# Optimization experiments

Measured on AMD Instinct MI355X. Metric: run time of the kernel, lower is better.

## Reference

```python
import jax, jax.numpy as jnp
import numpy as np
from jax.scipy.special import logsumexp

EPS = 1e-12  # torch F.normalize eps
SINKHORN_ITERS = 3


def _l2norm(a, axis):
    n = jnp.sqrt(jnp.sum(a * a, axis=axis, keepdims=True))
    return a / jnp.maximum(n, EPS)


def _log_optimal_transport(scores, alpha, iters):
    # scores: [B, m, n]; alpha: scalar dust-bin param
    b, m, n = scores.shape
    bins = jnp.broadcast_to(alpha, (b, 1, n)).astype(scores.dtype)
    Z = jnp.concatenate([scores, bins], axis=1)  # [B, m+1, n]
    norm = -np.log(float(m + n))
    log_mu = jnp.asarray(
        np.concatenate([np.full(m, norm), [np.log(float(n - m)) + norm]]),
        scores.dtype,
    )  # [m+1]
    log_nu = jnp.full((n,), norm, scores.dtype)
    u = jnp.zeros((b, m + 1), scores.dtype)
    v = jnp.zeros((b, n), scores.dtype)
    for _ in range(iters):
        u = log_mu[None, :] - logsumexp(Z + v[:, None, :], axis=2)
        v = log_nu[None, :] - logsumexp(Z + u[:, :, None], axis=1)
    return Z + u[:, :, None] + v[:, None, :] - norm


def _forward(x, t, tw1, tb1, tw2, tb2, cw1, cb1, cw2, cb2, sw1, sb1, sw2, sb2, dust_bin):
    B, C = x.shape[0], x.shape[1]
    xf = x.reshape(B, C, -1)  # [B, C, N], 1x1 convs act per-location
    # cluster features f: [B, l, N]
    h = jax.nn.relu(jnp.einsum('oc,bcn->bon', cw1, xf) + cb1[None, :, None])
    f = jnp.einsum('oc,bcn->bon', cw2, h) + cb2[None, :, None]
    # global token: [B, g]
    tok = jax.nn.relu(t @ tw1.T + tb1) @ tw2.T + tb2
    # assignment scores p: [B, m, N]
    hs = jax.nn.relu(jnp.einsum('oc,bcn->bon', sw1, xf) + sb1[None, :, None])
    p = jnp.einsum('oc,bcn->bon', sw2, hs) + sb2[None, :, None]
    Z = _log_optimal_transport(p, dust_bin, SINKHORN_ITERS)
    P = jnp.exp(Z)[:, :-1, :]  # drop dust bin row -> [B, m, N]
    # VLAD-style aggregation: the repeat/multiply/sum is just a batched matmul
    agg = jnp.einsum('bln,bmn->blm', f, P)  # [B, l, m]
    agg = _l2norm(agg, axis=1).reshape(B, -1)  # intra-normalize over l, flatten l-major
    out = jnp.concatenate([_l2norm(tok, axis=-1), agg], axis=-1)
    return _l2norm(out, axis=-1)


def setup_inputs() -> dict:
    key = jax.random.key(0)
    ks = jax.random.split(key, 14)
    B, C, H, W = 64, 768, 32, 32
    L, M, G, HID = 128, 64, 256, 512

    def p(k, shape):
        return jax.random.normal(k, shape, jnp.float32) * 0.02

    return {
        'x': jax.random.normal(ks[0], (B, C, H, W), jnp.float32),
        't': jax.random.normal(ks[1], (B, C), jnp.float32),
        'tw1': p(ks[2], (HID, C)), 'tb1': jnp.zeros((HID,), jnp.float32),
        'tw2': p(ks[3], (G, HID)), 'tb2': jnp.zeros((G,), jnp.float32),
        'cw1': p(ks[4], (HID, C)), 'cb1': jnp.zeros((HID,), jnp.float32),
        'cw2': p(ks[5], (L, HID)), 'cb2': jnp.zeros((L,), jnp.float32),
        'sw1': p(ks[6], (HID, C)), 'sb1': jnp.zeros((HID,), jnp.float32),
        'sw2': p(ks[7], (M, HID)), 'sb2': jnp.zeros((M,), jnp.float32),
        'dust_bin': jnp.asarray(1.0, jnp.float32),
    }


def reference(x, t, tw1, tb1, tw2, tb2, cw1, cb1, cw2, cb2, sw1, sb1, sw2, sb2, dust_bin):
    return _forward(x, t, tw1, tb1, tw2, tb2, cw1, cb1, cw2, cb2, sw1, sb1, sw2, sb2, dust_bin)
```

## Files before the change

### kernel.cpp

```cpp
#include <hip/hip_runtime.h>
#include <math.h>


#define B_SZ   64
#define C_IN   768
#define N_LOC  1024
#define HID    512
#define L_DIM  128
#define M_DIM  64
#define G_DIM  256

typedef unsigned short u16;
typedef __bf16 bf16x8 __attribute__((ext_vector_type(8)));
typedef float f32x4 __attribute__((ext_vector_type(4)));

typedef const __attribute__((address_space(1))) void* gptr_t;
typedef __attribute__((address_space(3))) void* sptr_t;

__device__ __forceinline__ void load_lds16(const void* g, void* l) {
    __builtin_amdgcn_global_load_lds((gptr_t)g, (sptr_t)l, 16, 0, 0);
}

__device__ __forceinline__ u16 f2bf(float f) {
    unsigned u = __float_as_uint(f);
    u += 0x7fffu + ((u >> 16) & 1u);
    return (u16)(u >> 16);
}
__device__ __forceinline__ float bf2f(u16 h) {
    return __uint_as_float(((unsigned)h) << 16);
}

__device__ __forceinline__ float waveReduceSum(float v) {
#pragma unroll
    for (int off = 32; off > 0; off >>= 1) v += __shfl_xor(v, off, 64);
    return v;
}

__global__ __launch_bounds__(256) void prep_weights(
        const float* __restrict__ cw1, const float* __restrict__ sw1,
        const float* __restrict__ cw2, const float* __restrict__ sw2,
        u16* __restrict__ cw1p, u16* __restrict__ sw1p,
        u16* __restrict__ cw2p, u16* __restrict__ sw2p) {
    const int q = blockIdx.x * 256 + threadIdx.x;
    const float* src;
    u16* dst;
    if (q < 98304) {
        int path = q / 49152, r = q % 49152;
        int kch = r / 512, c = r & 511;
        src = (path ? sw1 : cw1) + (size_t)c * C_IN + kch * 8;
        dst = (path ? sw1p : cw1p) + (size_t)r * 8;
    } else {
        int q2 = q - 98304;
        int path = (q2 >= 8192) ? 1 : 0;
        int r = q2 - (path ? 8192 : 0);
        int S2 = path ? M_DIM : L_DIM;
        int k2 = r / (4 * S2), kc = (r / S2) & 3, c = r % S2;
        src = (path ? sw2 : cw2) + (size_t)c * HID + k2 * 32 + kc * 8;
        dst = (path ? sw2p : cw2p) + (size_t)r * 8;
    }
    float4 v0 = *(const float4*)(src);
    float4 v1 = *(const float4*)(src + 4);
    *(ushort4*)(dst) = make_ushort4(f2bf(v0.x), f2bf(v0.y), f2bf(v0.z), f2bf(v0.w));
    *(ushort4*)(dst + 4) = make_ushort4(f2bf(v1.x), f2bf(v1.y), f2bf(v1.z), f2bf(v1.w));
}

__global__ __launch_bounds__(256) void transpose_x(const float* __restrict__ x,
                                                   u16* __restrict__ xP) {
    __shared__ float tile[64][65];
    const int n0 = blockIdx.x * 64;
    const int c0 = blockIdx.y * 64;
    const size_t b = blockIdx.z;
    const float* xb = x + b * (size_t)(C_IN * N_LOC);
    u16* xpb = xP + b * (size_t)(N_LOC * C_IN);
    const int tid = threadIdx.x;

    const int jn = (tid & 15) * 4;
    const int cr = tid >> 4;
#pragma unroll
    for (int r = 0; r < 4; ++r) {
        int c = cr + r * 16;
        float4 v = *(const float4*)(xb + (size_t)(c0 + c) * N_LOC + n0 + jn);
        tile[c][jn + 0] = v.x;
        tile[c][jn + 1] = v.y;
        tile[c][jn + 2] = v.z;
        tile[c][jn + 3] = v.w;
    }
    __syncthreads();

    const int n = tid & 63;
    const int ch0 = tid >> 6;
    const int nG = n0 + n;
#pragma unroll
    for (int r = 0; r < 2; ++r) {
        const int ch = ch0 + r * 4;
        const int cG = c0 + ch * 8;
        u16* dst = xpb + (size_t)(nG >> 7) * (128 * C_IN) + (cG >> 3) * 1024 +
                   (nG & 127) * 8;
        ushort4 o0 = make_ushort4(f2bf(tile[ch * 8 + 0][n]), f2bf(tile[ch * 8 + 1][n]),
                                  f2bf(tile[ch * 8 + 2][n]), f2bf(tile[ch * 8 + 3][n]));
        ushort4 o1 = make_ushort4(f2bf(tile[ch * 8 + 4][n]), f2bf(tile[ch * 8 + 5][n]),
                                  f2bf(tile[ch * 8 + 6][n]), f2bf(tile[ch * 8 + 7][n]));
        *(ushort4*)(dst) = o0;
        *(ushort4*)(dst + 4) = o1;
    }
}

__global__ __launch_bounds__(512, 2) void fused12(
        const u16* __restrict__ xP,
        const u16* __restrict__ cw1p, const float* __restrict__ cb1,
        const u16* __restrict__ cw2p, const float* __restrict__ cb2,
        const u16* __restrict__ sw1p, const float* __restrict__ sb1,
        const u16* __restrict__ sw2p, const float* __restrict__ sb2,
        u16* __restrict__ fT, u16* __restrict__ pT) {
    __shared__ __align__(16) u16 LDSu[81920];
    const int tid = threadIdx.x;
    const int lane = tid & 63;
    const int wid = tid >> 6;
    const int wr = wid >> 2;
    const int wc = wid & 3;

    const int id = blockIdx.x + 8 * blockIdx.y + 16 * blockIdx.z;
    const int nid = (id & 7) * 128 + (id >> 3);
    const int bx = nid & 7;
    const int path = (nid >> 3) & 1;
    const int bz = nid >> 4;
    const int r0 = bx * 128;

    const u16* W1p = path ? sw1p : cw1p;
    const float* B1 = path ? sb1 : cb1;
    const u16* W2p = path ? sw2p : cw2p;
    const float* B2 = path ? sb2 : cb2;
    u16* O2 = path ? pT : fT;
    const int S2 = path ? M_DIM : L_DIM;

    const u16* Ap = xP + (size_t)bz * N_LOC * C_IN + (size_t)bx * (128 * C_IN);

    f32x4 acc1[4][8];
#pragma unroll
    for (int mi = 0; mi < 4; ++mi)
#pragma unroll
        for (int ni = 0; ni < 8; ++ni)
            acc1[mi][ni] = (f32x4){0.f, 0.f, 0.f, 0.f};

    const int nk = C_IN / 64;

#define STG_A(db_, kt_)                                                        \
    do {                                                                       \
        _Pragma("unroll")                                                      \
        for (int j_ = 0; j_ < 2; ++j_)                                         \
            load_lds16(Ap + (size_t)(kt_) * 8192 + (size_t)(j_ * 512 + tid) * 8, \
                       &LDSu[(db_) * 8192 + (j_ * 512 + tid) * 8]);            \
    } while (0)
#define STG_B(db_, kt_)                                                        \
    do {                                                                       \
        _Pragma("unroll")                                                      \
        for (int j_ = 0; j_ < 8; ++j_)                                         \
            load_lds16(W1p + (size_t)(kt_) * 32768 + (size_t)(j_ * 512 + tid) * 8, \
                       &LDSu[16384 + (db_) * 32768 + (j_ * 512 + tid) * 8]);   \
    } while (0)

#define AV_PTR(db_, kk_, mi_)                                                  \
    ((const bf16x8*)&LDSu[(db_) * 8192 + ((kk_) * 4 + (lane >> 4)) * 1024 +    \
                          (64 * wr + 16 * (mi_) + (lane & 15)) * 8])
#define BW_PTR(db_, kk_, ni_)                                                  \
    ((const bf16x8*)&LDSu[16384 + (db_) * 32768 +                              \
                          ((kk_) * 4 + (lane >> 4)) * 4096 +                   \
                          (128 * wc + 16 * (ni_) + (lane & 15)) * 8])

#define PHASE_MID()                                                            \
    __builtin_amdgcn_s_barrier();                                              \
    asm volatile("s_waitcnt lgkmcnt(0)" ::: "memory");                         \
    __builtin_amdgcn_sched_barrier(0);                                         \
    __builtin_amdgcn_s_setprio(1)

#define PHASE_END()                                                            \
    __builtin_amdgcn_s_setprio(0);                                             \
    __builtin_amdgcn_sched_barrier(0);                                         \
    __builtin_amdgcn_s_barrier()

    STG_A(0, 0);
    STG_B(0, 0);
    asm volatile("s_waitcnt vmcnt(0)" ::: "memory");
    __builtin_amdgcn_s_barrier();

    for (int t = 0; t < nk; ++t) {
        const int db = t & 1;
        bf16x8 av[4], bw[8];

#pragma unroll
        for (int mi = 0; mi < 4; ++mi) av[mi] = *AV_PTR(db, 0, mi);
#pragma unroll
        for (int ni = 0; ni < 8; ++ni) bw[ni] = *BW_PTR(db, 0, ni);
        if (t + 1 < nk) {
            STG_B(db ^ 1, t + 1);
            STG_A(db ^ 1, t + 1);
        }
        PHASE_MID();
#pragma unroll
        for (int mi = 0; mi < 4; ++mi)
#pragma unroll
            for (int ni = 0; ni < 8; ++ni)
                acc1[mi][ni] = __builtin_amdgcn_mfma_f32_16x16x32_bf16(
                    av[mi], bw[ni], acc1[mi][ni], 0, 0, 0);
        PHASE_END();

#pragma unroll
        for (int mi = 0; mi < 4; ++mi) av[mi] = *AV_PTR(db, 1, mi);
#pragma unroll
        for (int ni = 0; ni < 8; ++ni) bw[ni] = *BW_PTR(db, 1, ni);
        PHASE_MID();
#pragma unroll
        for (int mi = 0; mi < 4; ++mi)
#pragma unroll
            for (int ni = 0; ni < 8; ++ni)
                acc1[mi][ni] = __builtin_amdgcn_mfma_f32_16x16x32_bf16(
                    av[mi], bw[ni], acc1[mi][ni], 0, 0, 0);
        __builtin_amdgcn_s_setprio(0);
        __builtin_amdgcn_sched_barrier(0);
        asm volatile("s_waitcnt vmcnt(0)" ::: "memory");
        __builtin_amdgcn_s_barrier();
    }
#undef STG_A
#undef STG_B
#undef AV_PTR
#undef BW_PTR
#undef PHASE_MID
#undef PHASE_END

    {
        float bv1[8];
#pragma unroll
        for (int ni = 0; ni < 8; ++ni)
            bv1[ni] = B1[128 * wc + 16 * ni + (lane & 15)];
#pragma unroll
        for (int mi = 0; mi < 4; ++mi)
#pragma unroll
            for (int ni = 0; ni < 8; ++ni)
#pragma unroll
                for (int rr = 0; rr < 4; ++rr) {
                    int n = 64 * wr + 16 * mi + (lane >> 4) * 4 + rr;
                    int c = 128 * wc + 16 * ni + (lane & 15);
                    float v = fmaxf(acc1[mi][ni][rr] + bv1[ni], 0.f);
                    LDSu[(c >> 3) * 1024 + n * 8 + (c & 7)] = f2bf(v);
                }
    }
    __syncthreads();

    f32x4 acc2[4][2];
#pragma unroll
    for (int mi = 0; mi < 4; ++mi) {
        acc2[mi][0] = (f32x4){0.f, 0.f, 0.f, 0.f};
        acc2[mi][1] = (f32x4){0.f, 0.f, 0.f, 0.f};
    }
    const int c2base = (S2 == L_DIM) ? 32 * wc : 16 * wc;
    const int cA = c2base + (lane & 15);
    const int cB = c2base + 16 + (lane & 15);
    const int fb0 = (lane >> 4) * S2 + cA;
    const int fb1 = (lane >> 4) * S2 + cB;

    bf16x8 w0n = *(const bf16x8*)(W2p + (size_t)fb0 * 8);
    bf16x8 w1n = {};
    if (S2 == L_DIM) w1n = *(const bf16x8*)(W2p + (size_t)fb1 * 8);

    for (int k2 = 0; k2 < 16; ++k2) {
        bf16x8 w0 = w0n, w1 = w1n;
        if (k2 < 15) {
            w0n = *(const bf16x8*)(W2p + ((size_t)(k2 + 1) * 4 * S2 + fb0) * 8);
            if (S2 == L_DIM)
                w1n = *(const bf16x8*)(W2p + ((size_t)(k2 + 1) * 4 * S2 + fb1) * 8);
        }
        bf16x8 a2[4];
#pragma unroll
        for (int mi = 0; mi < 4; ++mi)
            a2[mi] = *(const bf16x8*)&LDSu[(k2 * 4 + (lane >> 4)) * 1024 +
                                           (64 * wr + 16 * mi + (lane & 15)) * 8];
#pragma unroll
        for (int mi = 0; mi < 4; ++mi) {
            acc2[mi][0] = __builtin_amdgcn_mfma_f32_16x16x32_bf16(
                a2[mi], w0, acc2[mi][0], 0, 0, 0);
            if (S2 == L_DIM)
                acc2[mi][1] = __builtin_amdgcn_mfma_f32_16x16x32_bf16(
                    a2[mi], w1, acc2[mi][1], 0, 0, 0);
        }
    }

    const float b20 = B2[cA];
    const float b21 = (S2 == L_DIM) ? B2[cB] : 0.f;
    u16* Ob = O2 + (size_t)bz * N_LOC * S2;
#pragma unroll
    for (int mi = 0; mi < 4; ++mi)
#pragma unroll
        for (int rr = 0; rr < 4; ++rr) {
            int row = r0 + 64 * wr + 16 * mi + (lane >> 4) * 4 + rr;
            Ob[(size_t)row * S2 + cA] = f2bf(acc2[mi][0][rr] + b20);
            if (S2 == L_DIM)
                Ob[(size_t)row * S2 + cB] = f2bf(acc2[mi][1][rr] + b21);
        }
}

__global__ __launch_bounds__(256) void tok1_kernel(const float* __restrict__ t,
                                                   const float* __restrict__ tw1,
                                                   const float* __restrict__ tb1,
                                                   float* __restrict__ hidb) {
    __shared__ __align__(16) float tl[C_IN];
    const int b = blockIdx.y;
    const int j0 = blockIdx.x * 64;
    const int tid = threadIdx.x;
    const int lane = tid & 63;
    const int wave = tid >> 6;
    for (int i = tid; i < C_IN; i += 256) tl[i] = t[(size_t)b * C_IN + i];
    __syncthreads();
    for (int j = wave; j < 64; j += 4) {
        const int row = j0 + j;
        const float4* wr = (const float4*)(tw1 + (size_t)row * C_IN);
        const float4* tr = (const float4*)tl;
        float s = 0.f;
#pragma unroll
        for (int q = 0; q < 3; ++q) {
            float4 wv = wr[lane + 64 * q];
            float4 tv = tr[lane + 64 * q];
            s += wv.x * tv.x + wv.y * tv.y + wv.z * tv.z + wv.w * tv.w;
        }
        s = waveReduceSum(s);
        if (lane == 0) hidb[(size_t)b * HID + row] = fmaxf(s + tb1[row], 0.f);
    }
}

__global__ __launch_bounds__(256) void tok2_kernel(const float* __restrict__ hidb,
                                                   const float* __restrict__ tw2,
                                                   const float* __restrict__ tb2,
                                                   float* __restrict__ tok) {
    __shared__ __align__(16) float hl[HID];
    const int b = blockIdx.y;
    const int g0 = blockIdx.x * 64;
    const int tid = threadIdx.x;
    const int lane = tid & 63;
    const int wave = tid >> 6;
    for (int i = tid; i < HID; i += 256) hl[i] = hidb[(size_t)b * HID + i];
    __syncthreads();
    for (int j = wave; j < 64; j += 4) {
        const int row = g0 + j;
        const float4* wr = (const float4*)(tw2 + (size_t)row * HID);
        const float4* hr = (const float4*)hl;
        float s = 0.f;
#pragma unroll
        for (int q = 0; q < 2; ++q) {
            float4 wv = wr[lane + 64 * q];
            float4 hv = hr[lane + 64 * q];
            s += wv.x * hv.x + wv.y * hv.y + wv.z * hv.z + wv.w * hv.w;
        }
        s = waveReduceSum(s);
        if (lane == 0) tok[(size_t)b * G_DIM + row] = s + tb2[row];
    }
}

__global__ __launch_bounds__(1024) void sinkhorn_kernel(const u16* __restrict__ pT,
                                                        const float* __restrict__ dust,
                                                        float* __restrict__ PT) {
    __shared__ u16 sp[M_DIM][N_LOC];
    __shared__ float eu[M_DIM + 1];
    __shared__ float ev[N_LOC];
    const int b = blockIdx.x;
    const int t = threadIdx.x;
    const int lane = t & 63;
    const int wave = t >> 6;
    const float alpha = dust[0];
    const float Ea = __expf(alpha);
    const float mu = 1.f / 1088.f;
    const float mu64 = 960.f / 1088.f;
    const float nu = 1.f / 1088.f;

    const uint4* prow = (const uint4*)(pT + ((size_t)b * N_LOC + t) * M_DIM);
#pragma unroll
    for (int q = 0; q < 8; ++q) {
        uint4 ch = prow[q];
        sp[q * 8 + 0][t] = (u16)(ch.x);
        sp[q * 8 + 1][t] = (u16)(ch.x >> 16);
        sp[q * 8 + 2][t] = (u16)(ch.y);
        sp[q * 8 + 3][t] = (u16)(ch.y >> 16);
        sp[q * 8 + 4][t] = (u16)(ch.z);
        sp[q * 8 + 5][t] = (u16)(ch.z >> 16);
        sp[q * 8 + 6][t] = (u16)(ch.w);
        sp[q * 8 + 7][t] = (u16)(ch.w >> 16);
    }
#pragma unroll
    for (int m = 0; m < M_DIM; ++m)
        sp[m][t] = f2bf(__expf(bf2f(sp[m][t])));
    ev[t] = 1.f;
    __syncthreads();

    for (int it = 0; it < 3; ++it) {
        for (int m = wave; m < M_DIM + 1; m += 16) {
            float s = 0.f;
            if (m < M_DIM) {
#pragma unroll
                for (int q = 0; q < 16; ++q) {
                    int c = lane + 64 * q;
                    s += bf2f(sp[m][c]) * ev[c];
                }
            } else {
#pragma unroll
                for (int q = 0; q < 16; ++q) {
                    int c = lane + 64 * q;
                    s += ev[c];
                }
                s *= Ea;
            }
            s = waveReduceSum(s);
            if (lane == 0) eu[m] = ((m < M_DIM) ? mu : mu64) / s;
        }
        __syncthreads();
        float s = Ea * eu[M_DIM];
#pragma unroll 8
        for (int m = 0; m < M_DIM; ++m) s += bf2f(sp[m][t]) * eu[m];
        ev[t] = nu / s;
        __syncthreads();
    }

    const float evt = ev[t] * 1088.f;
    float* Prow = PT + ((size_t)b * N_LOC + t) * M_DIM;
#pragma unroll
    for (int m4 = 0; m4 < M_DIM; m4 += 4) {
        float4 o;
        o.x = bf2f(sp[m4 + 0][t]) * eu[m4 + 0] * evt;
        o.y = bf2f(sp[m4 + 1][t]) * eu[m4 + 1] * evt;
        o.z = bf2f(sp[m4 + 2][t]) * eu[m4 + 2] * evt;
        o.w = bf2f(sp[m4 + 3][t]) * eu[m4 + 3] * evt;
        *(float4*)(Prow + m4) = o;
    }
}

__global__ __launch_bounds__(256) void agg_kernel(const u16* __restrict__ fT,
                                                  const float* __restrict__ PT,
                                                  float* __restrict__ agg) {
    __shared__ float Fs[64][36];
    __shared__ float Ps[64][68];
    const int b = blockIdx.y;
    const int l0 = blockIdx.x * 32;
    const int tid = threadIdx.x;
    const u16* fb = fT + (size_t)b * N_LOC * L_DIM;
    const float* Pb = PT + (size_t)b * N_LOC * M_DIM;

    const int sn = tid >> 2;
    const int flc = (tid & 3) * 8;
    const int pmc = (tid & 3) * 16;
    const int tl = (tid >> 4) * 2;
    const int tm = (tid & 15) * 4;

    float acc[2][4] = {};

    for (int n0 = 0; n0 < N_LOC; n0 += 64) {
        __syncthreads();
        {
            uint4 ld = *(const uint4*)(fb + (size_t)(n0 + sn) * L_DIM + l0 + flc);
            Fs[sn][flc + 0] = bf2f((u16)(ld.x));
            Fs[sn][flc + 1] = bf2f((u16)(ld.x >> 16));
            Fs[sn][flc + 2] = bf2f((u16)(ld.y));
            Fs[sn][flc + 3] = bf2f((u16)(ld.y >> 16));
            Fs[sn][flc + 4] = bf2f((u16)(ld.z));
            Fs[sn][flc + 5] = bf2f((u16)(ld.z >> 16));
            Fs[sn][flc + 6] = bf2f((u16)(ld.w));
            Fs[sn][flc + 7] = bf2f((u16)(ld.w >> 16));
        }
#pragma unroll
        for (int i = 0; i < 4; ++i) {
            float4 vv = *(const float4*)(Pb + (size_t)(n0 + sn) * M_DIM + pmc + 4 * i);
            *(float4*)&Ps[sn][pmc + 4 * i] = vv;
        }
        __syncthreads();
#pragma unroll 8
        for (int nn = 0; nn < 64; ++nn) {
            float a0 = Fs[nn][tl];
            float a1 = Fs[nn][tl + 1];
            float4 p4 = *(const float4*)&Ps[nn][tm];
            acc[0][0] = fmaf(a0, p4.x, acc[0][0]);
            acc[0][1] = fmaf(a0, p4.y, acc[0][1]);
            acc[0][2] = fmaf(a0, p4.z, acc[0][2]);
            acc[0][3] = fmaf(a0, p4.w, acc[0][3]);
            acc[1][0] = fmaf(a1, p4.x, acc[1][0]);
            acc[1][1] = fmaf(a1, p4.y, acc[1][1]);
            acc[1][2] = fmaf(a1, p4.z, acc[1][2]);
            acc[1][3] = fmaf(a1, p4.w, acc[1][3]);
        }
    }

#pragma unroll
    for (int i = 0; i < 2; ++i) {
        float* dst = agg + ((size_t)b * L_DIM + l0 + tl + i) * M_DIM + tm;
        *(float4*)dst = make_float4(acc[i][0], acc[i][1], acc[i][2], acc[i][3]);
    }
}

__global__ __launch_bounds__(256) void final_kernel(const float* __restrict__ agg,
                                                    const float* __restrict__ tok,
                                                    float* __restrict__ out) {
    __shared__ __align__(16) float ag[L_DIM * M_DIM];
    __shared__ float rm[M_DIM];
    __shared__ float red[4];
    __shared__ float tk[G_DIM];
    const int b = blockIdx.x;
    const int tid = threadIdx.x;
    const int lane = tid & 63;
    const int wave = tid >> 6;
    const float EPS = 1e-12f;

    const float4* ab = (const float4*)(agg + (size_t)b * L_DIM * M_DIM);
    for (int e4 = tid; e4 < L_DIM * M_DIM / 4; e4 += 256) ((float4*)ag)[e4] = ab[e4];
    tk[tid] = tok[(size_t)b * G_DIM + tid];
    __syncthreads();

    if (tid < M_DIM) {
        float ss = 0.f;
#pragma unroll 8
        for (int l = 0; l < L_DIM; ++l) {
            float x = ag[l * M_DIM + tid];
            ss = fmaf(x, x, ss);
        }
        rm[tid] = 1.f / fmaxf(sqrtf(ss), EPS);
    }
    const float tv = tk[tid];
    float ssl = tv * tv;
    ssl = waveReduceSum(ssl);
    if (lane == 0) red[wave] = ssl;
    __syncthreads();
    const float stok = red[0] + red[1] + red[2] + red[3];
    const float rt = 1.f / fmaxf(sqrtf(stok), EPS);
    const float tn = tv * rt;

    float gs = tn * tn;
    for (int e = tid; e < L_DIM * M_DIM; e += 256) {
        float x = ag[e] * rm[e & (M_DIM - 1)];
        gs = fmaf(x, x, gs);
    }
    __syncthreads();
    gs = waveReduceSum(gs);
    if (lane == 0) red[wave] = gs;
    __syncthreads();
    const float G = red[0] + red[1] + red[2] + red[3];
    const float rg = 1.f / fmaxf(sqrtf(G), EPS);

    float* ob = out + (size_t)b * (G_DIM + L_DIM * M_DIM);
    ob[tid] = tn * rg;
    for (int e = tid; e < L_DIM * M_DIM; e += 256)
        ob[G_DIM + e] = ag[e] * rm[e & (M_DIM - 1)] * rg;
}

extern "C" void kernel_launch(void* const* d_in, const int* in_sizes, int n_in,
                              void* d_out, int out_size, void* d_ws, size_t ws_size,
                              hipStream_t stream) {
    const float* x    = (const float*)d_in[0];
    const float* t    = (const float*)d_in[1];
    const float* tw1  = (const float*)d_in[2];
    const float* tb1  = (const float*)d_in[3];
    const float* tw2  = (const float*)d_in[4];
    const float* tb2  = (const float*)d_in[5];
    const float* cw1  = (const float*)d_in[6];
    const float* cb1  = (const float*)d_in[7];
    const float* cw2  = (const float*)d_in[8];
    const float* cb2  = (const float*)d_in[9];
    const float* sw1  = (const float*)d_in[10];
    const float* sb1  = (const float*)d_in[11];
    const float* sw2  = (const float*)d_in[12];
    const float* sb2  = (const float*)d_in[13];
    const float* dust = (const float*)d_in[14];
    float* out = (float*)d_out;

    char* ws = (char*)d_ws;
    u16* xP    = (u16*)(ws);
    u16* fT    = (u16*)(ws + 100663296ull);
    u16* pT    = (u16*)(ws + 117440512ull);
    u16* cw1p  = (u16*)(ws + 125829120ull);
    u16* sw1p  = (u16*)(ws + 126615552ull);
    u16* cw2p  = (u16*)(ws + 127401984ull);
    u16* sw2p  = (u16*)(ws + 127533056ull);
    float* hidb = (float*)(ws + 127598592ull);
    float* PT     = (float*)(ws);
    float* tokbuf = (float*)(ws + 20971520ull);
    float* aggbuf = (float*)(ws + 25165824ull);

    prep_weights<<<432, 256, 0, stream>>>(cw1, sw1, cw2, sw2,
                                          cw1p, sw1p, cw2p, sw2p);
    transpose_x<<<dim3(N_LOC / 64, C_IN / 64, B_SZ), 256, 0, stream>>>(x, xP);

    fused12<<<dim3(8, 2, B_SZ), 512, 0, stream>>>(
        xP, cw1p, cb1, cw2p, cb2, sw1p, sb1, sw2p, sb2, fT, pT);

    tok1_kernel<<<dim3(HID / 64, B_SZ), 256, 0, stream>>>(t, tw1, tb1, hidb);
    tok2_kernel<<<dim3(G_DIM / 64, B_SZ), 256, 0, stream>>>(hidb, tw2, tb2, tokbuf);

    sinkhorn_kernel<<<B_SZ, 1024, 0, stream>>>(pT, dust, PT);
    agg_kernel<<<dim3(L_DIM / 32, B_SZ), 256, 0, stream>>>(fT, PT, aggbuf);
    final_kernel<<<B_SZ, 256, 0, stream>>>(aggbuf, tokbuf, out);
}
```

Before: 291.5 us.

## Shrink first GEMM K-tile with triple-buffered A and store transport plan as bf16

The first fused GEMM stage now uses K-tiles of 32 instead of 64, with a smaller LDS footprint. The activation tile is prefetched two steps ahead while the weight tile is double-buffered, and the loop uses one barrier pair per step instead of two phases. Separately, the Sinkhorn kernel writes the transport plan in bf16 instead of fp32, halving that intermediate's traffic into the aggregation kernel. The risks are more loop iterations and barriers per K, plus reduced precision in the transport plan.

```diff
diff --git a/kernel.cpp b/kernel.cpp
--- a/kernel.cpp
+++ b/kernel.cpp
@@ -112,7 +112,7 @@
         const u16* __restrict__ sw1p, const float* __restrict__ sb1,
         const u16* __restrict__ sw2p, const float* __restrict__ sb2,
         u16* __restrict__ fT, u16* __restrict__ pT) {
-    __shared__ __align__(16) u16 LDSu[81920];
+    __shared__ __align__(16) u16 LDSu[65536];
     const int tid = threadIdx.x;
     const int lane = tid & 63;
     const int wid = tid >> 6;
@@ -142,45 +142,29 @@
         for (int ni = 0; ni < 8; ++ni)
             acc1[mi][ni] = (f32x4){0.f, 0.f, 0.f, 0.f};
 
-    const int nk = C_IN / 64;
+    const int nk = C_IN / 32;
 
 #define STG_A(db_, kt_)                                                        \
-    do {                                                                       \
-        _Pragma("unroll")                                                      \
-        for (int j_ = 0; j_ < 2; ++j_)                                         \
-            load_lds16(Ap + (size_t)(kt_) * 8192 + (size_t)(j_ * 512 + tid) * 8, \
-                       &LDSu[(db_) * 8192 + (j_ * 512 + tid) * 8]);            \
-    } while (0)
+    load_lds16(Ap + (size_t)(kt_) * 4096 + tid * 8, &LDSu[(db_) * 4096 + tid * 8])
 #define STG_B(db_, kt_)                                                        \
     do {                                                                       \
         _Pragma("unroll")                                                      \
-        for (int j_ = 0; j_ < 8; ++j_)                                         \
-            load_lds16(W1p + (size_t)(kt_) * 32768 + (size_t)(j_ * 512 + tid) * 8, \
-                       &LDSu[16384 + (db_) * 32768 + (j_ * 512 + tid) * 8]);   \
+        for (int j_ = 0; j_ < 4; ++j_)                                         \
+            load_lds16(W1p + (size_t)(kt_) * 16384 + (size_t)(j_ * 512 + tid) * 8, \
+                       &LDSu[8192 + (db_) * 16384 + (j_ * 512 + tid) * 8]);    \
     } while (0)
 
-#define AV_PTR(db_, kk_, mi_)                                                  \
-    ((const bf16x8*)&LDSu[(db_) * 8192 + ((kk_) * 4 + (lane >> 4)) * 1024 +    \
+#define AV_PTR(db_, mi_)                                                       \
+    ((const bf16x8*)&LDSu[(db_) * 4096 + (lane >> 4) * 1024 +                  \
                           (64 * wr + 16 * (mi_) + (lane & 15)) * 8])
-#define BW_PTR(db_, kk_, ni_)                                                  \
-    ((const bf16x8*)&LDSu[16384 + (db_) * 32768 +                              \
-                          ((kk_) * 4 + (lane >> 4)) * 4096 +                   \
+#define BW_PTR(db_, ni_)                                                       \
+    ((const bf16x8*)&LDSu[8192 + (db_) * 16384 + (lane >> 4) * 4096 +          \
                           (128 * wc + 16 * (ni_) + (lane & 15)) * 8])
-
-#define PHASE_MID()                                                            \
-    __builtin_amdgcn_s_barrier();                                              \
-    asm volatile("s_waitcnt lgkmcnt(0)" ::: "memory");                         \
-    __builtin_amdgcn_sched_barrier(0);                                         \
-    __builtin_amdgcn_s_setprio(1)
-
-#define PHASE_END()                                                            \
-    __builtin_amdgcn_s_setprio(0);                                             \
-    __builtin_amdgcn_sched_barrier(0);                                         \
-    __builtin_amdgcn_s_barrier()
 
     STG_A(0, 0);
     STG_B(0, 0);
-    asm volatile("s_waitcnt vmcnt(0)" ::: "memory");
+    STG_A(1, 1);
+    asm volatile("s_waitcnt vmcnt(1)" ::: "memory");
     __builtin_amdgcn_s_barrier();
 
     for (int t = 0; t < nk; ++t) {
@@ -188,27 +172,18 @@
         bf16x8 av[4], bw[8];
 
 #pragma unroll
-        for (int mi = 0; mi < 4; ++mi) av[mi] = *AV_PTR(db, 0, mi);
-#pragma unroll
-        for (int ni = 0; ni < 8; ++ni) bw[ni] = *BW_PTR(db, 0, ni);
-        if (t + 1 < nk) {
-            STG_B(db ^ 1, t + 1);
-            STG_A(db ^ 1, t + 1);
-        }
-        PHASE_MID();
-#pragma unroll
-        for (int mi = 0; mi < 4; ++mi)
-#pragma unroll
-            for (int ni = 0; ni < 8; ++ni)
-                acc1[mi][ni] = __builtin_amdgcn_mfma_f32_16x16x32_bf16(
-                    av[mi], bw[ni], acc1[mi][ni], 0, 0, 0);
-        PHASE_END();
-
-#pragma unroll
-        for (int mi = 0; mi < 4; ++mi) av[mi] = *AV_PTR(db, 1, mi);
-#pragma unroll
-        for (int ni = 0; ni < 8; ++ni) bw[ni] = *BW_PTR(db, 1, ni);
-        PHASE_MID();
+        for (int mi = 0; mi < 4; ++mi) av[mi] = *AV_PTR(db, mi);
+#pragma unroll
+        for (int ni = 0; ni < 8; ++ni) bw[ni] = *BW_PTR(db, ni);
+        if (t + 1 < nk) STG_B(db ^ 1, t + 1);
+
+        asm volatile("s_waitcnt lgkmcnt(0)" ::: "memory");
+        __builtin_amdgcn_sched_barrier(0);
+        __builtin_amdgcn_s_barrier();
+
+        if (t + 2 < nk) STG_A(db, t + 2);
+
+        __builtin_amdgcn_s_setprio(1);
 #pragma unroll
         for (int mi = 0; mi < 4; ++mi)
 #pragma unroll
@@ -217,15 +192,17 @@
                     av[mi], bw[ni], acc1[mi][ni], 0, 0, 0);
         __builtin_amdgcn_s_setprio(0);
         __builtin_amdgcn_sched_barrier(0);
-        asm volatile("s_waitcnt vmcnt(0)" ::: "memory");
+
+        if (t + 2 < nk)
+            asm volatile("s_waitcnt vmcnt(1)" ::: "memory");
+        else
+            asm volatile("s_waitcnt vmcnt(0)" ::: "memory");
         __builtin_amdgcn_s_barrier();
     }
 #undef STG_A
 #undef STG_B
 #undef AV_PTR
 #undef BW_PTR
-#undef PHASE_MID
-#undef PHASE_END
 
     {
         float bv1[8];
@@ -356,7 +333,7 @@
 
 __global__ __launch_bounds__(1024) void sinkhorn_kernel(const u16* __restrict__ pT,
                                                         const float* __restrict__ dust,
-                                                        float* __restrict__ PT) {
+                                                        u16* __restrict__ PTb) {
     __shared__ u16 sp[M_DIM][N_LOC];
     __shared__ float eu[M_DIM + 1];
     __shared__ float ev[N_LOC];
@@ -418,20 +395,28 @@
     }
 
     const float evt = ev[t] * 1088.f;
-    float* Prow = PT + ((size_t)b * N_LOC + t) * M_DIM;
-#pragma unroll
-    for (int m4 = 0; m4 < M_DIM; m4 += 4) {
-        float4 o;
-        o.x = bf2f(sp[m4 + 0][t]) * eu[m4 + 0] * evt;
-        o.y = bf2f(sp[m4 + 1][t]) * eu[m4 + 1] * evt;
-        o.z = bf2f(sp[m4 + 2][t]) * eu[m4 + 2] * evt;
-        o.w = bf2f(sp[m4 + 3][t]) * eu[m4 + 3] * evt;
-        *(float4*)(Prow + m4) = o;
+    u16* Prow = PTb + ((size_t)b * N_LOC + t) * M_DIM;
+#pragma unroll
+    for (int m8 = 0; m8 < M_DIM; m8 += 8) {
+        unsigned v0 = f2bf(bf2f(sp[m8 + 0][t]) * eu[m8 + 0] * evt);
+        unsigned v1 = f2bf(bf2f(sp[m8 + 1][t]) * eu[m8 + 1] * evt);
+        unsigned v2 = f2bf(bf2f(sp[m8 + 2][t]) * eu[m8 + 2] * evt);
+        unsigned v3 = f2bf(bf2f(sp[m8 + 3][t]) * eu[m8 + 3] * evt);
+        unsigned v4 = f2bf(bf2f(sp[m8 + 4][t]) * eu[m8 + 4] * evt);
+        unsigned v5 = f2bf(bf2f(sp[m8 + 5][t]) * eu[m8 + 5] * evt);
+        unsigned v6 = f2bf(bf2f(sp[m8 + 6][t]) * eu[m8 + 6] * evt);
+        unsigned v7 = f2bf(bf2f(sp[m8 + 7][t]) * eu[m8 + 7] * evt);
+        uint4 w;
+        w.x = v0 | (v1 << 16);
+        w.y = v2 | (v3 << 16);
+        w.z = v4 | (v5 << 16);
+        w.w = v6 | (v7 << 16);
+        *(uint4*)(Prow + m8) = w;
     }
 }
 
 __global__ __launch_bounds__(256) void agg_kernel(const u16* __restrict__ fT,
-                                                  const float* __restrict__ PT,
+                                                  const u16* __restrict__ PTb,
                                                   float* __restrict__ agg) {
     __shared__ float Fs[64][36];
     __shared__ float Ps[64][68];
@@ -439,7 +424,7 @@
     const int l0 = blockIdx.x * 32;
     const int tid = threadIdx.x;
     const u16* fb = fT + (size_t)b * N_LOC * L_DIM;
-    const float* Pb = PT + (size_t)b * N_LOC * M_DIM;
+    const u16* Pb = PTb + (size_t)b * N_LOC * M_DIM;
 
     const int sn = tid >> 2;
     const int flc = (tid & 3) * 8;
@@ -462,10 +447,26 @@
             Fs[sn][flc + 6] = bf2f((u16)(ld.w));
             Fs[sn][flc + 7] = bf2f((u16)(ld.w >> 16));
         }
-#pragma unroll
-        for (int i = 0; i < 4; ++i) {
-            float4 vv = *(const float4*)(Pb + (size_t)(n0 + sn) * M_DIM + pmc + 4 * i);
-            *(float4*)&Ps[sn][pmc + 4 * i] = vv;
+        {
+            const u16* psrc = Pb + (size_t)(n0 + sn) * M_DIM + pmc;
+            uint4 p0 = *(const uint4*)(psrc);
+            uint4 p1 = *(const uint4*)(psrc + 8);
+            Ps[sn][pmc + 0] = bf2f((u16)(p0.x));
+            Ps[sn][pmc + 1] = bf2f((u16)(p0.x >> 16));
+            Ps[sn][pmc + 2] = bf2f((u16)(p0.y));
+            Ps[sn][pmc + 3] = bf2f((u16)(p0.y >> 16));
+            Ps[sn][pmc + 4] = bf2f((u16)(p0.z));
+            Ps[sn][pmc + 5] = bf2f((u16)(p0.z >> 16));
+            Ps[sn][pmc + 6] = bf2f((u16)(p0.w));
+            Ps[sn][pmc + 7] = bf2f((u16)(p0.w >> 16));
+            Ps[sn][pmc + 8] = bf2f((u16)(p1.x));
+            Ps[sn][pmc + 9] = bf2f((u16)(p1.x >> 16));
+            Ps[sn][pmc + 10] = bf2f((u16)(p1.y));
+            Ps[sn][pmc + 11] = bf2f((u16)(p1.y >> 16));
+            Ps[sn][pmc + 12] = bf2f((u16)(p1.z));
+            Ps[sn][pmc + 13] = bf2f((u16)(p1.z >> 16));
+            Ps[sn][pmc + 14] = bf2f((u16)(p1.w));
+            Ps[sn][pmc + 15] = bf2f((u16)(p1.w >> 16));
         }
         __syncthreads();
 #pragma unroll 8
@@ -574,7 +575,7 @@
     u16* cw2p  = (u16*)(ws + 127401984ull);
     u16* sw2p  = (u16*)(ws + 127533056ull);
     float* hidb = (float*)(ws + 127598592ull);
-    float* PT     = (float*)(ws);
+    u16* PTb      = (u16*)(ws);
     float* tokbuf = (float*)(ws + 20971520ull);
     float* aggbuf = (float*)(ws + 25165824ull);
 
@@ -588,7 +589,7 @@
     tok1_kernel<<<dim3(HID / 64, B_SZ), 256, 0, stream>>>(t, tw1, tb1, hidb);
     tok2_kernel<<<dim3(G_DIM / 64, B_SZ), 256, 0, stream>>>(hidb, tw2, tb2, tokbuf);
 
-    sinkhorn_kernel<<<B_SZ, 1024, 0, stream>>>(pT, dust, PT);
-    agg_kernel<<<dim3(L_DIM / 32, B_SZ), 256, 0, stream>>>(fT, PT, aggbuf);
+    sinkhorn_kernel<<<B_SZ, 1024, 0, stream>>>(pT, dust, PTb);
+    agg_kernel<<<dim3(L_DIM / 32, B_SZ), 256, 0, stream>>>(fT, PTb, aggbuf);
     final_kernel<<<B_SZ, 256, 0, stream>>>(aggbuf, tokbuf, out);
 }
```

After: 275.4 us. 1.06x faster.
